# Kernel tuning notes

Hardware: AMD Instinct MI355X
Metric: run time of the kernel (lower is better)

Reference implementation:

```python
import jax, jax.numpy as jnp
import numpy as np

B, S, D, H, O, E, TOPK = 4, 2048, 512, 1024, 512, 8, 2


def setup_inputs() -> dict:
    key = jax.random.key(0)
    ks = jax.random.split(key, 6)
    s = lambda d: 1.0 / np.sqrt(d)
    return {
        "x": jax.random.normal(ks[0], (B, S, D), dtype=jnp.float32),
        "Wg": jax.random.normal(ks[1], (D, E), dtype=jnp.float32) * s(D),
        "W1": jax.random.normal(ks[2], (E, D, H), dtype=jnp.float32) * s(D),
        "b1": jnp.zeros((E, H), dtype=jnp.float32),
        "W2": jax.random.normal(ks[3], (E, H, O), dtype=jnp.float32) * s(H),
        "b2": jnp.zeros((E, O), dtype=jnp.float32),
    }


def reference(x, Wg, W1, b1, W2, b2):
    Bsz, Seq, Din = x.shape
    T = Bsz * Seq
    xm = x.reshape(T, Din)                       # [T, D] token matrix
    # router: softmax over experts, then top-k (ProbabilitySamplerTopk)
    probs = jax.nn.softmax(xm @ Wg, axis=-1)     # [T, E]
    top_p, top_i = jax.lax.top_k(probs, TOPK)    # [T, k]
    # dense scattered gates (topKProbabilitiesScattered in _computeGating);
    # zero entries for non-selected experts make the einsum combine exactly
    # equal to the original gather->per-expert-GEMM->index_add pipeline.
    gates = jnp.zeros((T, E), dtype=probs.dtype).at[
        jnp.arange(T)[:, None], top_i
    ].set(top_p)                                 # [T, E]
    # per-expert 2-layer MLP (inputExperts -> activation -> outputExperts)
    h = jax.nn.gelu(jnp.einsum("td,edh->teh", xm, W1) + b1[None])  # [T, E, H]
    y = jnp.einsum("teh,eho->teo", h, W2) + b2[None]               # [T, E, O]
    # weighted combine (multiply_by_gates + index_add)
    out = jnp.einsum("te,teo->to", gates, y)     # [T, O]
    return out.reshape(Bsz, Seq, O)
```

## Files before the change

### kernel.cpp

```cpp
#include <hip/hip_runtime.h>

#define T_TOK 8192
#define DIM   512
#define HID   1024
#define OUTD  512
#define NE    8

typedef __attribute__((ext_vector_type(8))) short short8v;
typedef __attribute__((ext_vector_type(4))) float f32x4;

__device__ __forceinline__ unsigned short f2bf(float f) {
  unsigned int u = __builtin_bit_cast(unsigned int, f);
  u += 0x7fffu + ((u >> 16) & 1u);
  return (unsigned short)(u >> 16);
}

__device__ __forceinline__ float bf2f(unsigned short h) {
  unsigned int u = ((unsigned int)h) << 16;
  return __builtin_bit_cast(float, u);
}

__device__ __forceinline__ void gload_lds16(const void* g, void* l) {
  __builtin_amdgcn_global_load_lds(
      (__attribute__((address_space(1))) void*)g,
      (__attribute__((address_space(3))) void*)l, 16, 0, 0);
}

__device__ __forceinline__ float gelu_f(float v) {
  const float c0 = 0.7978845608028654f;
  float u = c0 * (v + 0.044715f * v * v * v);
  return v / (1.0f + __expf(-2.0f * u));
}

__global__ __launch_bounds__(256) void k_trans_all(
    const float* __restrict__ W1, const float* __restrict__ W2,
    unsigned short* __restrict__ W1t, unsigned short* __restrict__ W2t) {
  __shared__ float tile[32][33];
  int bid = blockIdx.x;
  int which = bid >> 12;
  int r = bid & 4095;
  int e = r >> 9;
  int t = r & 511;
  int R = which ? HID : DIM;
  int C = which ? OUTD : HID;
  int tx, ty;
  if (which == 0) { ty = t >> 5; tx = t & 31; }
  else            { ty = t >> 4; tx = t & 15; }
  const float* inE = (which ? W2 : W1) + (size_t)e * R * C;
  unsigned short* outE = (which ? W2t : W1t) + (size_t)e * R * C;
  int c0 = tx * 32, r0 = ty * 32;
  int x = threadIdx.x, y = threadIdx.y;
#pragma unroll
  for (int i = 0; i < 32; i += 8)
    tile[y + i][x] = inE[(size_t)(r0 + y + i) * C + (c0 + x)];
  __syncthreads();
#pragma unroll
  for (int i = 0; i < 32; i += 8)
    outE[(size_t)(c0 + y + i) * R + (r0 + x)] = f2bf(tile[x][y + i]);
}

__global__ __launch_bounds__(256) void k_router(
    const float* __restrict__ x, const float* __restrict__ Wg,
    int* __restrict__ top_e, float* __restrict__ top_p) {
  int lane = threadIdx.x & 63;
  int t = blockIdx.x * 4 + (threadIdx.x >> 6);
  const float* xr = x + (size_t)t * DIM;
  int j0 = lane * 8;
  float4 xa = *(const float4*)(xr + j0);
  float4 xb = *(const float4*)(xr + j0 + 4);
  float xl[8] = {xa.x, xa.y, xa.z, xa.w, xb.x, xb.y, xb.z, xb.w};
  float acc[8] = {0.f,0.f,0.f,0.f,0.f,0.f,0.f,0.f};
#pragma unroll
  for (int jj = 0; jj < 8; ++jj) {
    float4 w0 = *(const float4*)(Wg + (size_t)(j0 + jj) * NE);
    float4 w1 = *(const float4*)(Wg + (size_t)(j0 + jj) * NE + 4);
    acc[0] += xl[jj] * w0.x; acc[1] += xl[jj] * w0.y;
    acc[2] += xl[jj] * w0.z; acc[3] += xl[jj] * w0.w;
    acc[4] += xl[jj] * w1.x; acc[5] += xl[jj] * w1.y;
    acc[6] += xl[jj] * w1.z; acc[7] += xl[jj] * w1.w;
  }
#pragma unroll
  for (int off = 32; off >= 1; off >>= 1) {
#pragma unroll
    for (int e2 = 0; e2 < 8; ++e2) acc[e2] += __shfl_xor(acc[e2], off, 64);
  }
  if (lane == 0) {
    float m = acc[0];
#pragma unroll
    for (int e2 = 1; e2 < 8; ++e2) m = fmaxf(m, acc[e2]);
    float p[8]; float s = 0.f;
#pragma unroll
    for (int e2 = 0; e2 < 8; ++e2) { p[e2] = expf(acc[e2] - m); s += p[e2]; }
    float inv = 1.f / s;
    int i0 = 0;
#pragma unroll
    for (int e2 = 1; e2 < 8; ++e2) if (p[e2] > p[i0]) i0 = e2;
    int i1 = (i0 == 0) ? 1 : 0;
#pragma unroll
    for (int e2 = 0; e2 < 8; ++e2) if (e2 != i0 && p[e2] > p[i1]) i1 = e2;
    top_e[t * 2] = i0;  top_e[t * 2 + 1] = i1;
    top_p[t * 2] = p[i0] * inv;  top_p[t * 2 + 1] = p[i1] * inv;
  }
}

__global__ __launch_bounds__(256) void k_plan(
    const int* __restrict__ top_e, int* __restrict__ localRank,
    int* __restrict__ blockCounts) {
  __shared__ int cnt[4][NE];
  __shared__ int wbase[4][NE];
  int tid = threadIdx.x, lane = tid & 63, w = tid >> 6;
  int a = blockIdx.x * 256 + tid;
  int e = top_e[a];
  int rank = 0;
#pragma unroll
  for (int e2 = 0; e2 < NE; ++e2) {
    unsigned long long m = __ballot(e == e2);
    if (e == e2) rank = __popcll(m & ((1ULL << lane) - 1ULL));
    if (lane == 0) cnt[w][e2] = __popcll(m);
  }
  __syncthreads();
  if (tid < NE) {
    int s = 0;
#pragma unroll
    for (int w2 = 0; w2 < 4; ++w2) { wbase[w2][tid] = s; s += cnt[w2][tid]; }
    blockCounts[blockIdx.x * NE + tid] = s;
  }
  __syncthreads();
  localRank[a] = wbase[w][e] + rank;
}

__global__ void k_scan2(const int* __restrict__ blockCounts, int* __restrict__ baseBlk,
                        int* __restrict__ offs, int nBlocks) {
  __shared__ int tot[NE];
  int tid = threadIdx.x;
  if (tid < NE) {
    int s = 0;
    for (int b = 0; b < nBlocks; ++b) { baseBlk[b * NE + tid] = s; s += blockCounts[b * NE + tid]; }
    tot[tid] = s;
  }
  __syncthreads();
  if (tid == 0) {
    int s = 0;
    for (int e = 0; e < NE; ++e) { offs[e] = s; s += tot[e]; }
    offs[NE] = s;
  }
}

__global__ __launch_bounds__(256) void k_scatter(
    const float* __restrict__ x, const int* __restrict__ top_e,
    const int* __restrict__ localRank, const int* __restrict__ baseBlk,
    const int* __restrict__ offs, int* __restrict__ pos_of,
    unsigned short* __restrict__ Xp) {
  int lane = threadIdx.x & 63;
  int a = blockIdx.x * 4 + (threadIdx.x >> 6);
  int t = a >> 1;
  int e = top_e[a];
  int pos = offs[e] + baseBlk[(a >> 8) * NE + e] + localRank[a];
  if (lane == 0) pos_of[a] = pos;
  const float* xr = x + (size_t)t * DIM + lane * 8;
  float4 xa = *(const float4*)xr;
  float4 xb = *(const float4*)(xr + 4);
  short8v pk;
  pk[0] = (short)f2bf(xa.x); pk[1] = (short)f2bf(xa.y);
  pk[2] = (short)f2bf(xa.z); pk[3] = (short)f2bf(xa.w);
  pk[4] = (short)f2bf(xb.x); pk[5] = (short)f2bf(xb.y);
  pk[6] = (short)f2bf(xb.z); pk[7] = (short)f2bf(xb.w);
  *(short8v*)(Xp + (size_t)pos * DIM + lane * 8) = pk;
}

#define MFMA1(d, a, b) d = __builtin_amdgcn_mfma_f32_16x16x32_bf16(a, b, d, 0, 0, 0)

template<int NX, int LOG2NX, int EPI>
__global__ __launch_bounds__(256, 4) void k_gemm_x(
    const unsigned short* __restrict__ A, const unsigned short* __restrict__ Bt,
    const float* __restrict__ bias, const int* __restrict__ offs,
    unsigned short* __restrict__ Hout, unsigned short* __restrict__ Ybf,
    int K, int N) {
  __shared__ __align__(16) unsigned short Al[128 * 64];
  __shared__ __align__(16) unsigned short Bl[128 * 64];

  const int e = blockIdx.x & 7;
  const int slot = blockIdx.x >> 3;
  const int nSlots = gridDim.x >> 3;
  const int rowBeg = offs[e], rowEnd = offs[e + 1];
  if (rowBeg >= rowEnd) return;
  const int nMT = (rowEnd - rowBeg + 127) >> 7;
  const int nWork = nMT << LOG2NX;
  const unsigned short* Be = Bt + (size_t)e * N * K;

  const int tid = threadIdx.x, lane = tid & 63, w = tid >> 6;
  const int wr = w >> 1, wc = w & 1;
  const int fr = lane & 15, fq = lane >> 4;
  const int sRow = tid >> 3;
  const int sCe = ((((tid & 7) << 4) ^ ((sRow & 7) << 4)) >> 1);
  const int NT = K >> 6;

  for (int idx = slot; idx < nWork; idx += nSlots) {
    const int mt = idx >> LOG2NX;
    const int xb = idx & (NX - 1);
    const int m0 = rowBeg + mt * 128;
    const int n0 = xb * 128;

    const char* aP[4]; const char* bP[4];
#pragma unroll
    for (int c_ = 0; c_ < 4; ++c_) {
      int ar_ = m0 + c_ * 32 + sRow; if (ar_ > rowEnd - 1) ar_ = rowEnd - 1;
      aP[c_] = (const char*)(A + (size_t)ar_ * K + sCe);
      int br_ = n0 + c_ * 32 + sRow;
      bP[c_] = (const char*)(Be + (size_t)br_ * K + sCe);
    }

    f32x4 acc[4][4];
#pragma unroll
    for (int m = 0; m < 4; ++m)
#pragma unroll
      for (int n = 0; n < 4; ++n) acc[m][n] = (f32x4){0.f, 0.f, 0.f, 0.f};

    for (int t = 0; t < NT; ++t) {
      const int tOff = t << 7;
#pragma unroll
      for (int c_ = 0; c_ < 4; ++c_)
        gload_lds16(aP[c_] + tOff, (char*)&Al[0] + c_ * 4096 + (w << 10));
#pragma unroll
      for (int c_ = 0; c_ < 4; ++c_)
        gload_lds16(bP[c_] + tOff, (char*)&Bl[0] + c_ * 4096 + (w << 10));
      __syncthreads();
#pragma unroll
      for (int kk = 0; kk < 2; ++kk) {
        short8v av[4], bv[4];
#pragma unroll
        for (int m = 0; m < 4; ++m) {
          int row_ = wr * 64 + m * 16 + fr;
          av[m] = *(const short8v*)((const char*)&Al[0] + row_ * 128 +
                    (((kk << 6) + (fq << 4)) ^ ((fr & 7) << 4)));
        }
#pragma unroll
        for (int n = 0; n < 4; ++n) {
          int row_ = wc * 64 + n * 16 + fr;
          bv[n] = *(const short8v*)((const char*)&Bl[0] + row_ * 128 +
                    (((kk << 6) + (fq << 4)) ^ ((fr & 7) << 4)));
        }
#pragma unroll
        for (int m = 0; m < 4; ++m)
#pragma unroll
          for (int n = 0; n < 4; ++n)
            MFMA1(acc[m][n], av[m], bv[n]);
      }
      __syncthreads();
    }

#pragma unroll
    for (int m = 0; m < 4; ++m) {
#pragma unroll
      for (int j = 0; j < 4; ++j) {
        int row = m0 + wr * 64 + m * 16 + fq * 4 + j;
        if (row >= rowEnd) continue;
#pragma unroll
        for (int n = 0; n < 4; ++n) {
          int col = n0 + wc * 64 + n * 16 + fr;
          float v = acc[m][n][j] + bias[(size_t)e * N + col];
          if (EPI == 0) Hout[(size_t)row * N + col] = f2bf(gelu_f(v));
          else          Ybf[(size_t)row * N + col] = f2bf(v);
        }
      }
    }
  }
}

template<int NX, int LOG2NX, int EPI>
__global__ __launch_bounds__(512, 4) void k_gemm_w(
    const unsigned short* __restrict__ A, const unsigned short* __restrict__ Bt,
    const float* __restrict__ bias, const int* __restrict__ offs,
    unsigned short* __restrict__ Hout, unsigned short* __restrict__ Ybf,
    int K, int N) {
  __shared__ __align__(16) unsigned short Al[256 * 64];
  __shared__ __align__(16) unsigned short Bl[128 * 64];

  const int e = blockIdx.x & 7;
  const int slot = blockIdx.x >> 3;
  const int nSlots = gridDim.x >> 3;
  const int rowBeg = offs[e], rowEnd = offs[e + 1];
  if (rowBeg >= rowEnd) return;
  const int nMT = (rowEnd - rowBeg + 255) >> 8;
  const int nWork = nMT << LOG2NX;
  const unsigned short* Be = Bt + (size_t)e * N * K;

  const int tid = threadIdx.x, lane = tid & 63, w = tid >> 6;
  const int wm = w >> 1, wn = w & 1;
  const int fr = lane & 15, fq = lane >> 4;
  const int sRow = tid >> 3;
  const int sCe = ((((tid & 7) << 4) ^ ((sRow & 7) << 4)) >> 1);
  const int NT = K >> 6;

  for (int idx = slot; idx < nWork; idx += nSlots) {
    const int mt = idx >> LOG2NX;
    const int xb = idx & (NX - 1);
    const int m0 = rowBeg + mt * 256;
    const int n0 = xb * 128;

    const char* aP[4]; const char* bP[2];
#pragma unroll
    for (int c_ = 0; c_ < 4; ++c_) {
      int ar_ = m0 + c_ * 64 + sRow; if (ar_ > rowEnd - 1) ar_ = rowEnd - 1;
      aP[c_] = (const char*)(A + (size_t)ar_ * K + sCe);
    }
#pragma unroll
    for (int c_ = 0; c_ < 2; ++c_) {
      int br_ = n0 + c_ * 64 + sRow;
      bP[c_] = (const char*)(Be + (size_t)br_ * K + sCe);
    }

    f32x4 acc[4][4];
#pragma unroll
    for (int m = 0; m < 4; ++m)
#pragma unroll
      for (int n = 0; n < 4; ++n) acc[m][n] = (f32x4){0.f, 0.f, 0.f, 0.f};

    for (int t = 0; t < NT; ++t) {
      const int tOff = t << 7;
#pragma unroll
      for (int c_ = 0; c_ < 4; ++c_)
        gload_lds16(aP[c_] + tOff, (char*)&Al[0] + c_ * 8192 + (w << 10));
#pragma unroll
      for (int c_ = 0; c_ < 2; ++c_)
        gload_lds16(bP[c_] + tOff, (char*)&Bl[0] + c_ * 8192 + (w << 10));
      __syncthreads();
#pragma unroll
      for (int kk = 0; kk < 2; ++kk) {
        short8v av[4], bv[4];
#pragma unroll
        for (int m = 0; m < 4; ++m) {
          int row_ = wm * 64 + m * 16 + fr;
          av[m] = *(const short8v*)((const char*)&Al[0] + row_ * 128 +
                    (((kk << 6) + (fq << 4)) ^ ((fr & 7) << 4)));
        }
#pragma unroll
        for (int n = 0; n < 4; ++n) {
          int row_ = wn * 64 + n * 16 + fr;
          bv[n] = *(const short8v*)((const char*)&Bl[0] + row_ * 128 +
                    (((kk << 6) + (fq << 4)) ^ ((fr & 7) << 4)));
        }
#pragma unroll
        for (int m = 0; m < 4; ++m)
#pragma unroll
          for (int n = 0; n < 4; ++n)
            MFMA1(acc[m][n], av[m], bv[n]);
      }
      __syncthreads();
    }

#pragma unroll
    for (int m = 0; m < 4; ++m) {
#pragma unroll
      for (int j = 0; j < 4; ++j) {
        int row = m0 + wm * 64 + m * 16 + fq * 4 + j;
        if (row >= rowEnd) continue;
#pragma unroll
        for (int n = 0; n < 4; ++n) {
          int col = n0 + wn * 64 + n * 16 + fr;
          float v = acc[m][n][j] + bias[(size_t)e * N + col];
          if (EPI == 0) Hout[(size_t)row * N + col] = f2bf(gelu_f(v));
          else          Ybf[(size_t)row * N + col] = f2bf(v);
        }
      }
    }
  }
}

__global__ __launch_bounds__(256) void k_combine(
    const unsigned short* __restrict__ Y, const int* __restrict__ pos_of,
    const float* __restrict__ top_p, float* __restrict__ out) {
  int lane = threadIdx.x & 63;
  int t = blockIdx.x * 4 + (threadIdx.x >> 6);
  int p0 = pos_of[t * 2], p1 = pos_of[t * 2 + 1];
  float g0 = top_p[t * 2], g1 = top_p[t * 2 + 1];
  short8v ya = *(const short8v*)(Y + (size_t)p0 * OUTD + lane * 8);
  short8v yb = *(const short8v*)(Y + (size_t)p1 * OUTD + lane * 8);
  float4 r0, r1;
  r0.x = g0 * bf2f((unsigned short)ya[0]) + g1 * bf2f((unsigned short)yb[0]);
  r0.y = g0 * bf2f((unsigned short)ya[1]) + g1 * bf2f((unsigned short)yb[1]);
  r0.z = g0 * bf2f((unsigned short)ya[2]) + g1 * bf2f((unsigned short)yb[2]);
  r0.w = g0 * bf2f((unsigned short)ya[3]) + g1 * bf2f((unsigned short)yb[3]);
  r1.x = g0 * bf2f((unsigned short)ya[4]) + g1 * bf2f((unsigned short)yb[4]);
  r1.y = g0 * bf2f((unsigned short)ya[5]) + g1 * bf2f((unsigned short)yb[5]);
  r1.z = g0 * bf2f((unsigned short)ya[6]) + g1 * bf2f((unsigned short)yb[6]);
  r1.w = g0 * bf2f((unsigned short)ya[7]) + g1 * bf2f((unsigned short)yb[7]);
  float4* o = (float4*)(out + (size_t)t * OUTD + lane * 8);
  o[0] = r0; o[1] = r1;
}

extern "C" void kernel_launch(void* const* d_in, const int* in_sizes, int n_in,
                              void* d_out, int out_size, void* d_ws, size_t ws_size,
                              hipStream_t stream) {
  const float* x  = (const float*)d_in[0];
  const float* Wg = (const float*)d_in[1];
  const float* W1 = (const float*)d_in[2];
  const float* b1 = (const float*)d_in[3];
  const float* W2 = (const float*)d_in[4];
  const float* b2 = (const float*)d_in[5];
  float* out = (float*)d_out;

  char* p = (char*)d_ws;
  auto take = [&](size_t bytes) { char* r = p; p += (bytes + 255) & ~(size_t)255; return r; };
  unsigned short* W1t = (unsigned short*)take((size_t)NE * DIM * HID * 2);
  unsigned short* W2t = (unsigned short*)take((size_t)NE * HID * OUTD * 2);
  unsigned short* Xp  = (unsigned short*)take((size_t)2 * T_TOK * DIM * 2);
  unsigned short* Hb  = (unsigned short*)take((size_t)2 * T_TOK * HID * 2);
  unsigned short* Yb  = (unsigned short*)take((size_t)2 * T_TOK * OUTD * 2);
  int* offs   = (int*)take(4096);
  int*   top_e  = (int*)take((size_t)2 * T_TOK * 4);
  float* top_pv = (float*)take((size_t)2 * T_TOK * 4);
  int*   pos_of = (int*)take((size_t)2 * T_TOK * 4);
  int* localRank   = (int*)take((size_t)2 * T_TOK * 4);
  int* blockCounts = (int*)take((size_t)64 * NE * 4);
  int* baseBlk     = (int*)take((size_t)64 * NE * 4);

  const int PLAN_BLOCKS = (2 * T_TOK) / 256;

  k_trans_all<<<8192, dim3(32, 8), 0, stream>>>(W1, W2, W1t, W2t);
  k_router<<<T_TOK / 4, 256, 0, stream>>>(x, Wg, top_e, top_pv);
  k_plan<<<PLAN_BLOCKS, 256, 0, stream>>>(top_e, localRank, blockCounts);
  k_scan2<<<1, 64, 0, stream>>>(blockCounts, baseBlk, offs, PLAN_BLOCKS);
  k_scatter<<<(2 * T_TOK) / 4, 256, 0, stream>>>(x, top_e, localRank, baseBlk, offs, pos_of, Xp);
  k_gemm_w<8, 3, 0><<<1024, 512, 0, stream>>>(Xp, W1t, b1, offs, Hb, nullptr, DIM, HID);
  k_gemm_x<4, 2, 1><<<512, 256, 0, stream>>>(Hb, W2t, b2, offs, nullptr, Yb, HID, OUTD);
  k_combine<<<T_TOK / 4, 256, 0, stream>>>(Yb, pos_of, top_pv, out);
}
```

Measured before the change: 137.7 us.

## Merge transpose and router kernels, fold scan into scatter, deepen K tile

Result: faster. 126.9 us, median of 2 (-7.8%).

```diff
diff --git a/kernel.cpp b/kernel.cpp
--- a/kernel.cpp
+++ b/kernel.cpp
@@ -32,74 +32,75 @@
   return v / (1.0f + __expf(-2.0f * u));
 }
 
-__global__ __launch_bounds__(256) void k_trans_all(
+__global__ __launch_bounds__(256) void k_prep(
     const float* __restrict__ W1, const float* __restrict__ W2,
-    unsigned short* __restrict__ W1t, unsigned short* __restrict__ W2t) {
-  __shared__ float tile[32][33];
-  int bid = blockIdx.x;
-  int which = bid >> 12;
-  int r = bid & 4095;
-  int e = r >> 9;
-  int t = r & 511;
-  int R = which ? HID : DIM;
-  int C = which ? OUTD : HID;
-  int tx, ty;
-  if (which == 0) { ty = t >> 5; tx = t & 31; }
-  else            { ty = t >> 4; tx = t & 15; }
-  const float* inE = (which ? W2 : W1) + (size_t)e * R * C;
-  unsigned short* outE = (which ? W2t : W1t) + (size_t)e * R * C;
-  int c0 = tx * 32, r0 = ty * 32;
-  int x = threadIdx.x, y = threadIdx.y;
-#pragma unroll
-  for (int i = 0; i < 32; i += 8)
-    tile[y + i][x] = inE[(size_t)(r0 + y + i) * C + (c0 + x)];
-  __syncthreads();
-#pragma unroll
-  for (int i = 0; i < 32; i += 8)
-    outE[(size_t)(c0 + y + i) * R + (r0 + x)] = f2bf(tile[x][y + i]);
-}
-
-__global__ __launch_bounds__(256) void k_router(
+    unsigned short* __restrict__ W1t, unsigned short* __restrict__ W2t,
     const float* __restrict__ x, const float* __restrict__ Wg,
     int* __restrict__ top_e, float* __restrict__ top_p) {
-  int lane = threadIdx.x & 63;
-  int t = blockIdx.x * 4 + (threadIdx.x >> 6);
-  const float* xr = x + (size_t)t * DIM;
-  int j0 = lane * 8;
-  float4 xa = *(const float4*)(xr + j0);
-  float4 xb = *(const float4*)(xr + j0 + 4);
-  float xl[8] = {xa.x, xa.y, xa.z, xa.w, xb.x, xb.y, xb.z, xb.w};
-  float acc[8] = {0.f,0.f,0.f,0.f,0.f,0.f,0.f,0.f};
-#pragma unroll
-  for (int jj = 0; jj < 8; ++jj) {
-    float4 w0 = *(const float4*)(Wg + (size_t)(j0 + jj) * NE);
-    float4 w1 = *(const float4*)(Wg + (size_t)(j0 + jj) * NE + 4);
-    acc[0] += xl[jj] * w0.x; acc[1] += xl[jj] * w0.y;
-    acc[2] += xl[jj] * w0.z; acc[3] += xl[jj] * w0.w;
-    acc[4] += xl[jj] * w1.x; acc[5] += xl[jj] * w1.y;
-    acc[6] += xl[jj] * w1.z; acc[7] += xl[jj] * w1.w;
-  }
-#pragma unroll
-  for (int off = 32; off >= 1; off >>= 1) {
-#pragma unroll
-    for (int e2 = 0; e2 < 8; ++e2) acc[e2] += __shfl_xor(acc[e2], off, 64);
-  }
-  if (lane == 0) {
-    float m = acc[0];
-#pragma unroll
-    for (int e2 = 1; e2 < 8; ++e2) m = fmaxf(m, acc[e2]);
-    float p[8]; float s = 0.f;
-#pragma unroll
-    for (int e2 = 0; e2 < 8; ++e2) { p[e2] = expf(acc[e2] - m); s += p[e2]; }
-    float inv = 1.f / s;
-    int i0 = 0;
-#pragma unroll
-    for (int e2 = 1; e2 < 8; ++e2) if (p[e2] > p[i0]) i0 = e2;
-    int i1 = (i0 == 0) ? 1 : 0;
-#pragma unroll
-    for (int e2 = 0; e2 < 8; ++e2) if (e2 != i0 && p[e2] > p[i1]) i1 = e2;
-    top_e[t * 2] = i0;  top_e[t * 2 + 1] = i1;
-    top_p[t * 2] = p[i0] * inv;  top_p[t * 2 + 1] = p[i1] * inv;
+  int bid = blockIdx.x;
+  int tid = threadIdx.x;
+  if (bid < 8192) {
+    __shared__ float tile[32][33];
+    int which = bid >> 12;
+    int r = bid & 4095;
+    int e = r >> 9;
+    int t = r & 511;
+    int R = which ? HID : DIM;
+    int C = which ? OUTD : HID;
+    int tx, ty;
+    if (which == 0) { ty = t >> 5; tx = t & 31; }
+    else            { ty = t >> 4; tx = t & 15; }
+    const float* inE = (which ? W2 : W1) + (size_t)e * R * C;
+    unsigned short* outE = (which ? W2t : W1t) + (size_t)e * R * C;
+    int c0 = tx * 32, r0 = ty * 32;
+    int xx = tid & 31, yy = tid >> 5;
+#pragma unroll
+    for (int i = 0; i < 32; i += 8)
+      tile[yy + i][xx] = inE[(size_t)(r0 + yy + i) * C + (c0 + xx)];
+    __syncthreads();
+#pragma unroll
+    for (int i = 0; i < 32; i += 8)
+      outE[(size_t)(c0 + yy + i) * R + (r0 + xx)] = f2bf(tile[xx][yy + i]);
+  } else {
+    int lane = tid & 63;
+    int t = (bid - 8192) * 4 + (tid >> 6);
+    const float* xr = x + (size_t)t * DIM;
+    int j0 = lane * 8;
+    float4 xa = *(const float4*)(xr + j0);
+    float4 xb = *(const float4*)(xr + j0 + 4);
+    float xl[8] = {xa.x, xa.y, xa.z, xa.w, xb.x, xb.y, xb.z, xb.w};
+    float acc[8] = {0.f,0.f,0.f,0.f,0.f,0.f,0.f,0.f};
+#pragma unroll
+    for (int jj = 0; jj < 8; ++jj) {
+      float4 w0 = *(const float4*)(Wg + (size_t)(j0 + jj) * NE);
+      float4 w1 = *(const float4*)(Wg + (size_t)(j0 + jj) * NE + 4);
+      acc[0] += xl[jj] * w0.x; acc[1] += xl[jj] * w0.y;
+      acc[2] += xl[jj] * w0.z; acc[3] += xl[jj] * w0.w;
+      acc[4] += xl[jj] * w1.x; acc[5] += xl[jj] * w1.y;
+      acc[6] += xl[jj] * w1.z; acc[7] += xl[jj] * w1.w;
+    }
+#pragma unroll
+    for (int off = 32; off >= 1; off >>= 1) {
+#pragma unroll
+      for (int e2 = 0; e2 < 8; ++e2) acc[e2] += __shfl_xor(acc[e2], off, 64);
+    }
+    if (lane == 0) {
+      float m = acc[0];
+#pragma unroll
+      for (int e2 = 1; e2 < 8; ++e2) m = fmaxf(m, acc[e2]);
+      float p[8]; float s = 0.f;
+#pragma unroll
+      for (int e2 = 0; e2 < 8; ++e2) { p[e2] = expf(acc[e2] - m); s += p[e2]; }
+      float inv = 1.f / s;
+      int i0 = 0;
+#pragma unroll
+      for (int e2 = 1; e2 < 8; ++e2) if (p[e2] > p[i0]) i0 = e2;
+      int i1 = (i0 == 0) ? 1 : 0;
+#pragma unroll
+      for (int e2 = 0; e2 < 8; ++e2) if (e2 != i0 && p[e2] > p[i1]) i1 = e2;
+      top_e[t * 2] = i0;  top_e[t * 2 + 1] = i1;
+      top_p[t * 2] = p[i0] * inv;  top_p[t * 2 + 1] = p[i1] * inv;
+    }
   }
 }
 
@@ -129,33 +130,41 @@
   localRank[a] = wbase[w][e] + rank;
 }
 
-__global__ void k_scan2(const int* __restrict__ blockCounts, int* __restrict__ baseBlk,
-                        int* __restrict__ offs, int nBlocks) {
-  __shared__ int tot[NE];
+__global__ __launch_bounds__(256) void k_scatter(
+    const float* __restrict__ x, const int* __restrict__ top_e,
+    const int* __restrict__ localRank, const int* __restrict__ blockCounts,
+    int* __restrict__ offs, int* __restrict__ pos_of,
+    unsigned short* __restrict__ Xp) {
+  __shared__ int sBase[NE];
+  __shared__ int sTot[NE];
+  __shared__ int sOffs[NE];
   int tid = threadIdx.x;
+  int g = blockIdx.x >> 6;
   if (tid < NE) {
-    int s = 0;
-    for (int b = 0; b < nBlocks; ++b) { baseBlk[b * NE + tid] = s; s += blockCounts[b * NE + tid]; }
-    tot[tid] = s;
+    int pre = 0, tot = 0;
+    for (int b = 0; b < 64; ++b) {
+      int c = blockCounts[b * NE + tid];
+      if (b < g) pre += c;
+      tot += c;
+    }
+    sBase[tid] = pre; sTot[tid] = tot;
   }
   __syncthreads();
   if (tid == 0) {
     int s = 0;
-    for (int e = 0; e < NE; ++e) { offs[e] = s; s += tot[e]; }
-    offs[NE] = s;
-  }
-}
-
-__global__ __launch_bounds__(256) void k_scatter(
-    const float* __restrict__ x, const int* __restrict__ top_e,
-    const int* __restrict__ localRank, const int* __restrict__ baseBlk,
-    const int* __restrict__ offs, int* __restrict__ pos_of,
-    unsigned short* __restrict__ Xp) {
-  int lane = threadIdx.x & 63;
-  int a = blockIdx.x * 4 + (threadIdx.x >> 6);
+#pragma unroll
+    for (int e = 0; e < NE; ++e) { sOffs[e] = s; s += sTot[e]; }
+    if (blockIdx.x == 0) {
+      for (int e = 0; e < NE; ++e) offs[e] = sOffs[e];
+      offs[NE] = s;
+    }
+  }
+  __syncthreads();
+  int lane = tid & 63;
+  int a = blockIdx.x * 4 + (tid >> 6);
   int t = a >> 1;
   int e = top_e[a];
-  int pos = offs[e] + baseBlk[(a >> 8) * NE + e] + localRank[a];
+  int pos = sOffs[e] + sBase[e] + localRank[a];
   if (lane == 0) pos_of[a] = pos;
   const float* xr = x + (size_t)t * DIM + lane * 8;
   float4 xa = *(const float4*)xr;
@@ -170,14 +179,112 @@
 
 #define MFMA1(d, a, b) d = __builtin_amdgcn_mfma_f32_16x16x32_bf16(a, b, d, 0, 0, 0)
 
-template<int NX, int LOG2NX, int EPI>
-__global__ __launch_bounds__(256, 4) void k_gemm_x(
+template<int NX, int LOG2NX>
+__global__ __launch_bounds__(512, 4) void k_gemm_w(
     const unsigned short* __restrict__ A, const unsigned short* __restrict__ Bt,
     const float* __restrict__ bias, const int* __restrict__ offs,
-    unsigned short* __restrict__ Hout, unsigned short* __restrict__ Ybf,
-    int K, int N) {
-  __shared__ __align__(16) unsigned short Al[128 * 64];
+    unsigned short* __restrict__ Hout, int K, int N) {
+  __shared__ __align__(16) unsigned short Al[256 * 64];
   __shared__ __align__(16) unsigned short Bl[128 * 64];
+
+  const int e = blockIdx.x & 7;
+  const int slot = blockIdx.x >> 3;
+  const int nSlots = gridDim.x >> 3;
+  const int rowBeg = offs[e], rowEnd = offs[e + 1];
+  if (rowBeg >= rowEnd) return;
+  const int nMT = (rowEnd - rowBeg + 255) >> 8;
+  const int nWork = nMT << LOG2NX;
+  const unsigned short* Be = Bt + (size_t)e * N * K;
+
+  const int tid = threadIdx.x, lane = tid & 63, w = tid >> 6;
+  const int wm = w >> 1, wn = w & 1;
+  const int fr = lane & 15, fq = lane >> 4;
+  const int sRow = tid >> 3;
+  const int sCe = ((((tid & 7) << 4) ^ ((sRow & 7) << 4)) >> 1);
+  const int NT = K >> 6;
+
+  for (int idx = slot; idx < nWork; idx += nSlots) {
+    const int mt = idx >> LOG2NX;
+    const int xb = idx & (NX - 1);
+    const int m0 = rowBeg + mt * 256;
+    const int n0 = xb * 128;
+
+    const char* aP[4]; const char* bP[2];
+#pragma unroll
+    for (int c_ = 0; c_ < 4; ++c_) {
+      int ar_ = m0 + c_ * 64 + sRow; if (ar_ > rowEnd - 1) ar_ = rowEnd - 1;
+      aP[c_] = (const char*)(A + (size_t)ar_ * K + sCe);
+    }
+#pragma unroll
+    for (int c_ = 0; c_ < 2; ++c_) {
+      int br_ = n0 + c_ * 64 + sRow;
+      bP[c_] = (const char*)(Be + (size_t)br_ * K + sCe);
+    }
+
+    f32x4 acc[4][4];
+#pragma unroll
+    for (int m = 0; m < 4; ++m)
+#pragma unroll
+      for (int n = 0; n < 4; ++n) acc[m][n] = (f32x4){0.f, 0.f, 0.f, 0.f};
+
+    for (int t = 0; t < NT; ++t) {
+      const int tOff = t << 7;
+#pragma unroll
+      for (int c_ = 0; c_ < 4; ++c_)
+        gload_lds16(aP[c_] + tOff, (char*)&Al[0] + c_ * 8192 + (w << 10));
+#pragma unroll
+      for (int c_ = 0; c_ < 2; ++c_)
+        gload_lds16(bP[c_] + tOff, (char*)&Bl[0] + c_ * 8192 + (w << 10));
+      __syncthreads();
+#pragma unroll
+      for (int kk = 0; kk < 2; ++kk) {
+        short8v av[4], bv[4];
+#pragma unroll
+        for (int m = 0; m < 4; ++m) {
+          int row_ = wm * 64 + m * 16 + fr;
+          av[m] = *(const short8v*)((const char*)&Al[0] + row_ * 128 +
+                    (((kk << 6) + (fq << 4)) ^ ((fr & 7) << 4)));
+        }
+#pragma unroll
+        for (int n = 0; n < 4; ++n) {
+          int row_ = wn * 64 + n * 16 + fr;
+          bv[n] = *(const short8v*)((const char*)&Bl[0] + row_ * 128 +
+                    (((kk << 6) + (fq << 4)) ^ ((fr & 7) << 4)));
+        }
+#pragma unroll
+        for (int m = 0; m < 4; ++m)
+#pragma unroll
+          for (int n = 0; n < 4; ++n)
+            MFMA1(acc[m][n], av[m], bv[n]);
+      }
+      __syncthreads();
+    }
+
+#pragma unroll
+    for (int m = 0; m < 4; ++m) {
+#pragma unroll
+      for (int j = 0; j < 4; ++j) {
+        int row = m0 + wm * 64 + m * 16 + fq * 4 + j;
+        if (row >= rowEnd) continue;
+#pragma unroll
+        for (int n = 0; n < 4; ++n) {
+          int col = n0 + wn * 64 + n * 16 + fr;
+          float v = acc[m][n][j] + bias[(size_t)e * N + col];
+          Hout[(size_t)row * N + col] = f2bf(gelu_f(v));
+        }
+      }
+    }
+  }
+}
+
+template<int NX, int LOG2NX>
+__global__ __launch_bounds__(256, 2) void k_gemm_y(
+    const unsigned short* __restrict__ A,
+    const unsigned short* __restrict__ Bt,
+    const float* __restrict__ bias, const int* __restrict__ offs,
+    unsigned short* __restrict__ Ybf, int K, int N) {
+  __shared__ __align__(16) unsigned short Al[128 * 128];
+  __shared__ __align__(16) unsigned short Bl[128 * 128];
 
   const int e = blockIdx.x & 7;
   const int slot = blockIdx.x >> 3;
@@ -191,9 +298,9 @@
   const int tid = threadIdx.x, lane = tid & 63, w = tid >> 6;
   const int wr = w >> 1, wc = w & 1;
   const int fr = lane & 15, fq = lane >> 4;
-  const int sRow = tid >> 3;
-  const int sCe = ((((tid & 7) << 4) ^ ((sRow & 7) << 4)) >> 1);
-  const int NT = K >> 6;
+  const int sRow = tid >> 4;
+  const int sCb = (((tid & 15) << 4) ^ ((sRow & 7) << 4));
+  const int NT = K >> 7;
 
   for (int idx = slot; idx < nWork; idx += nSlots) {
     const int mt = idx >> LOG2NX;
@@ -201,14 +308,14 @@
     const int m0 = rowBeg + mt * 128;
     const int n0 = xb * 128;
 
-    const char* aP[4]; const char* bP[4];
-#pragma unroll
-    for (int c_ = 0; c_ < 4; ++c_) {
-      int ar_ = m0 + c_ * 32 + sRow; if (ar_ > rowEnd - 1) ar_ = rowEnd - 1;
-      aP[c_] = (const char*)(A + (size_t)ar_ * K + sCe);
-      int br_ = n0 + c_ * 32 + sRow;
-      bP[c_] = (const char*)(Be + (size_t)br_ * K + sCe);
-    }
+    const char* aP[8];
+#pragma unroll
+    for (int c_ = 0; c_ < 8; ++c_) {
+      int ar_ = m0 + c_ * 16 + sRow; if (ar_ > rowEnd - 1) ar_ = rowEnd - 1;
+      aP[c_] = (const char*)(A + (size_t)ar_ * K) + sCb;
+    }
+    const char* bP0 = (const char*)(Be + (size_t)(n0 + sRow) * K) + sCb;
+    const int bStride = 16 * K * 2;
 
     f32x4 acc[4][4];
 #pragma unroll
@@ -217,27 +324,27 @@
       for (int n = 0; n < 4; ++n) acc[m][n] = (f32x4){0.f, 0.f, 0.f, 0.f};
 
     for (int t = 0; t < NT; ++t) {
-      const int tOff = t << 7;
-#pragma unroll
-      for (int c_ = 0; c_ < 4; ++c_)
-        gload_lds16(aP[c_] + tOff, (char*)&Al[0] + c_ * 4096 + (w << 10));
-#pragma unroll
-      for (int c_ = 0; c_ < 4; ++c_)
-        gload_lds16(bP[c_] + tOff, (char*)&Bl[0] + c_ * 4096 + (w << 10));
+      const int tOff = t << 8;
+#pragma unroll
+      for (int c_ = 0; c_ < 8; ++c_)
+        gload_lds16(aP[c_] + tOff, (char*)&Al[0] + c_ * 4096 + (tid << 4));
+#pragma unroll
+      for (int c_ = 0; c_ < 8; ++c_)
+        gload_lds16(bP0 + c_ * bStride + tOff, (char*)&Bl[0] + c_ * 4096 + (tid << 4));
       __syncthreads();
 #pragma unroll
-      for (int kk = 0; kk < 2; ++kk) {
+      for (int kk = 0; kk < 4; ++kk) {
         short8v av[4], bv[4];
 #pragma unroll
         for (int m = 0; m < 4; ++m) {
           int row_ = wr * 64 + m * 16 + fr;
-          av[m] = *(const short8v*)((const char*)&Al[0] + row_ * 128 +
+          av[m] = *(const short8v*)((const char*)&Al[0] + row_ * 256 +
                     (((kk << 6) + (fq << 4)) ^ ((fr & 7) << 4)));
         }
 #pragma unroll
         for (int n = 0; n < 4; ++n) {
           int row_ = wc * 64 + n * 16 + fr;
-          bv[n] = *(const short8v*)((const char*)&Bl[0] + row_ * 128 +
+          bv[n] = *(const short8v*)((const char*)&Bl[0] + row_ * 256 +
                     (((kk << 6) + (fq << 4)) ^ ((fr & 7) << 4)));
         }
 #pragma unroll
@@ -259,108 +366,7 @@
         for (int n = 0; n < 4; ++n) {
           int col = n0 + wc * 64 + n * 16 + fr;
           float v = acc[m][n][j] + bias[(size_t)e * N + col];
-          if (EPI == 0) Hout[(size_t)row * N + col] = f2bf(gelu_f(v));
-          else          Ybf[(size_t)row * N + col] = f2bf(v);
-        }
-      }
-    }
-  }
-}
-
-template<int NX, int LOG2NX, int EPI>
-__global__ __launch_bounds__(512, 4) void k_gemm_w(
-    const unsigned short* __restrict__ A, const unsigned short* __restrict__ Bt,
-    const float* __restrict__ bias, const int* __restrict__ offs,
-    unsigned short* __restrict__ Hout, unsigned short* __restrict__ Ybf,
-    int K, int N) {
-  __shared__ __align__(16) unsigned short Al[256 * 64];
-  __shared__ __align__(16) unsigned short Bl[128 * 64];
-
-  const int e = blockIdx.x & 7;
-  const int slot = blockIdx.x >> 3;
-  const int nSlots = gridDim.x >> 3;
-  const int rowBeg = offs[e], rowEnd = offs[e + 1];
-  if (rowBeg >= rowEnd) return;
-  const int nMT = (rowEnd - rowBeg + 255) >> 8;
-  const int nWork = nMT << LOG2NX;
-  const unsigned short* Be = Bt + (size_t)e * N * K;
-
-  const int tid = threadIdx.x, lane = tid & 63, w = tid >> 6;
-  const int wm = w >> 1, wn = w & 1;
-  const int fr = lane & 15, fq = lane >> 4;
-  const int sRow = tid >> 3;
-  const int sCe = ((((tid & 7) << 4) ^ ((sRow & 7) << 4)) >> 1);
-  const int NT = K >> 6;
-
-  for (int idx = slot; idx < nWork; idx += nSlots) {
-    const int mt = idx >> LOG2NX;
-    const int xb = idx & (NX - 1);
-    const int m0 = rowBeg + mt * 256;
-    const int n0 = xb * 128;
-
-    const char* aP[4]; const char* bP[2];
-#pragma unroll
-    for (int c_ = 0; c_ < 4; ++c_) {
-      int ar_ = m0 + c_ * 64 + sRow; if (ar_ > rowEnd - 1) ar_ = rowEnd - 1;
-      aP[c_] = (const char*)(A + (size_t)ar_ * K + sCe);
-    }
-#pragma unroll
-    for (int c_ = 0; c_ < 2; ++c_) {
-      int br_ = n0 + c_ * 64 + sRow;
-      bP[c_] = (const char*)(Be + (size_t)br_ * K + sCe);
-    }
-
-    f32x4 acc[4][4];
-#pragma unroll
-    for (int m = 0; m < 4; ++m)
-#pragma unroll
-      for (int n = 0; n < 4; ++n) acc[m][n] = (f32x4){0.f, 0.f, 0.f, 0.f};
-
-    for (int t = 0; t < NT; ++t) {
-      const int tOff = t << 7;
-#pragma unroll
-      for (int c_ = 0; c_ < 4; ++c_)
-        gload_lds16(aP[c_] + tOff, (char*)&Al[0] + c_ * 8192 + (w << 10));
-#pragma unroll
-      for (int c_ = 0; c_ < 2; ++c_)
-        gload_lds16(bP[c_] + tOff, (char*)&Bl[0] + c_ * 8192 + (w << 10));
-      __syncthreads();
-#pragma unroll
-      for (int kk = 0; kk < 2; ++kk) {
-        short8v av[4], bv[4];
-#pragma unroll
-        for (int m = 0; m < 4; ++m) {
-          int row_ = wm * 64 + m * 16 + fr;
-          av[m] = *(const short8v*)((const char*)&Al[0] + row_ * 128 +
-                    (((kk << 6) + (fq << 4)) ^ ((fr & 7) << 4)));
-        }
-#pragma unroll
-        for (int n = 0; n < 4; ++n) {
-          int row_ = wn * 64 + n * 16 + fr;
-          bv[n] = *(const short8v*)((const char*)&Bl[0] + row_ * 128 +
-                    (((kk << 6) + (fq << 4)) ^ ((fr & 7) << 4)));
-        }
-#pragma unroll
-        for (int m = 0; m < 4; ++m)
-#pragma unroll
-          for (int n = 0; n < 4; ++n)
-            MFMA1(acc[m][n], av[m], bv[n]);
-      }
-      __syncthreads();
-    }
-
-#pragma unroll
-    for (int m = 0; m < 4; ++m) {
-#pragma unroll
-      for (int j = 0; j < 4; ++j) {
-        int row = m0 + wm * 64 + m * 16 + fq * 4 + j;
-        if (row >= rowEnd) continue;
-#pragma unroll
-        for (int n = 0; n < 4; ++n) {
-          int col = n0 + wn * 64 + n * 16 + fr;
-          float v = acc[m][n][j] + bias[(size_t)e * N + col];
-          if (EPI == 0) Hout[(size_t)row * N + col] = f2bf(gelu_f(v));
-          else          Ybf[(size_t)row * N + col] = f2bf(v);
+          Ybf[(size_t)row * N + col] = f2bf(v);
         }
       }
     }
@@ -413,16 +419,14 @@
   int*   pos_of = (int*)take((size_t)2 * T_TOK * 4);
   int* localRank   = (int*)take((size_t)2 * T_TOK * 4);
   int* blockCounts = (int*)take((size_t)64 * NE * 4);
-  int* baseBlk     = (int*)take((size_t)64 * NE * 4);
 
   const int PLAN_BLOCKS = (2 * T_TOK) / 256;
 
-  k_trans_all<<<8192, dim3(32, 8), 0, stream>>>(W1, W2, W1t, W2t);
-  k_router<<<T_TOK / 4, 256, 0, stream>>>(x, Wg, top_e, top_pv);
+  k_prep<<<8192 + 2048, 256, 0, stream>>>(W1, W2, W1t, W2t, x, Wg, top_e, top_pv);
   k_plan<<<PLAN_BLOCKS, 256, 0, stream>>>(top_e, localRank, blockCounts);
-  k_scan2<<<1, 64, 0, stream>>>(blockCounts, baseBlk, offs, PLAN_BLOCKS);
-  k_scatter<<<(2 * T_TOK) / 4, 256, 0, stream>>>(x, top_e, localRank, baseBlk, offs, pos_of, Xp);
-  k_gemm_w<8, 3, 0><<<1024, 512, 0, stream>>>(Xp, W1t, b1, offs, Hb, nullptr, DIM, HID);
-  k_gemm_x<4, 2, 1><<<512, 256, 0, stream>>>(Hb, W2t, b2, offs, nullptr, Yb, HID, OUTD);
+  k_scatter<<<(2 * T_TOK) / 4, 256, 0, stream>>>(x, top_e, localRank, blockCounts,
+                                                 offs, pos_of, Xp);
+  k_gemm_w<8, 3><<<1024, 512, 0, stream>>>(Xp, W1t, b1, offs, Hb, DIM, HID);
+  k_gemm_y<4, 2><<<512, 256, 0, stream>>>(Hb, W2t, b2, offs, Yb, HID, OUTD);
   k_combine<<<T_TOK / 4, 256, 0, stream>>>(Yb, pos_of, top_pv, out);
 }
```
